# Optimization experiments

Hardware: AMD Instinct MI355X
Metric: run time of the kernel (lower is better)

## Reference

```python
import jax, jax.numpy as jnp
import numpy as np

N = 50000        # n_nodes
F_IN = 256       # features_size
E_DIM = 128      # embedding_size
K = 2
N_FILT = 5
N_EDGES = 600000
EPS = 1e-9


def setup_inputs() -> dict:
    key = jax.random.key(0)
    ks = jax.random.split(key, 12)
    stdv = 1.0 / np.sqrt(E_DIM)  # matches torch reset_parameters / nn.Linear init scale
    feature = jax.random.normal(ks[0], (N, F_IN), dtype=jnp.float32)
    edge_index = jax.random.randint(ks[1], (2, N_EDGES), 0, N, dtype=jnp.int64)
    edge_weight = jax.random.uniform(ks[2], (N_EDGES,), dtype=jnp.float32)
    weight = jax.random.normal(ks[3], (F_IN, E_DIM), dtype=jnp.float32) * stdv
    low_gamma = jax.random.uniform(ks[4], (N_FILT, K), dtype=jnp.float32)
    mid_gamma = jax.random.uniform(ks[5], (N_FILT, K), dtype=jnp.float32)
    q_w = jax.random.normal(ks[6], (E_DIM, E_DIM), dtype=jnp.float32) * stdv
    q_b = jax.random.normal(ks[7], (E_DIM,), dtype=jnp.float32) * stdv
    k_w = jax.random.normal(ks[8], (E_DIM, E_DIM), dtype=jnp.float32) * stdv
    k_b = jax.random.normal(ks[9], (E_DIM,), dtype=jnp.float32) * stdv
    v_w = jax.random.normal(ks[10], (E_DIM, E_DIM), dtype=jnp.float32) * stdv
    v_b = jax.random.normal(ks[11], (E_DIM,), dtype=jnp.float32) * stdv
    return {"feature": feature, "edge_index": edge_index, "edge_weight": edge_weight,
            "weight": weight, "low_gamma": low_gamma, "mid_gamma": mid_gamma,
            "q_w": q_w, "q_b": q_b, "k_w": k_w, "k_b": k_b, "v_w": v_w, "v_b": v_b}


def reference(feature, edge_index, edge_weight, weight, low_gamma, mid_gamma,
              q_w, q_b, k_w, k_b, v_w, v_b):
    n = feature.shape[0]
    support = jax.nn.relu(feature @ weight)                     # [N, E]
    row, col = edge_index[0], edge_index[1]
    # torch.spmm(adj, support): adj_support[i] = sum_e w_e * support[col_e] for row_e == i
    adj_support = jax.ops.segment_sum(edge_weight[:, None] * support[col], row,
                                      num_segments=n)           # [N, E]

    alpha = jnp.linspace(jnp.float32(-EPS), jnp.float32(1.0 + EPS), K)  # [K]

    # low filters: out_i = dot(alpha, g_i) * adj_support + dot(1-alpha, g_i) * support, summed over i
    gl = jax.nn.relu(low_gamma)                                 # [5, K]
    a_low = jnp.sum(gl @ alpha)
    b_low = jnp.sum(gl @ (1.0 - alpha))
    output_low = a_low * adj_support + b_low * support          # [N, E]

    # mid filters: out_i = sum(g_i) * adj_support - dot(alpha, g_i) * support, summed over i
    gm = jax.nn.relu(mid_gamma)
    a_mid = jnp.sum(gm)
    c_mid = jnp.sum(gm @ alpha)
    output_mid = a_mid * adj_support - c_mid * support          # [N, E]

    # SelfAttention over the 2 filter outputs per node
    x = jnp.stack([output_low, output_mid], axis=1)             # [N, 2, E]
    q = x @ q_w.T + q_b
    k = x @ k_w.T + k_b
    v = x @ v_w.T + v_b
    scores = jnp.einsum('nqe,nke->nqk', q, k) / jnp.sqrt(jnp.float32(E_DIM))
    # NOTE: original uses nn.Softmax(dim=1) -> softmax over the QUERY axis
    w = jax.nn.softmax(scores, axis=1)                          # [N, 2, 2]
    context = jnp.einsum('nqk,nke->nqe', w, v)                  # [N, 2, E]
    return jnp.sum(context, axis=1)                             # [N, E]
```

## Files before the change

### kernel.cpp

```cpp
#include <hip/hip_runtime.h>
#include <hip/hip_bf16.h>

static constexpr int EDIM = 128;
static constexpr int FIN  = 256;
static constexpr int CAP  = 64;

typedef __attribute__((ext_vector_type(8))) short bf16x8;
typedef __attribute__((ext_vector_type(4))) float f32x4;

__device__ inline short f2b(float f) {
    __hip_bfloat16 h = __float2bfloat16(f);
    return *reinterpret_cast<short*>(&h);
}

__global__ __launch_bounds__(256) void k_prep(const float* __restrict__ W,
                                              const float* __restrict__ vw,
                                              const float* __restrict__ lg,
                                              const float* __restrict__ mg,
                                              short* __restrict__ WtF,
                                              short* __restrict__ vwF,
                                              float* __restrict__ sc,
                                              int* __restrict__ cnt, int M) {
    const int bid = blockIdx.x, tid = threadIdx.x;
    if (bid < 16) {
        int idx = bid * 256 + tid;
        int kt = idx >> 9, rem = idx & 511;
        int nf = rem >> 6, lane = rem & 63;
        int l15 = lane & 15, lhi = lane >> 4;
        bf16x8 fr;
        #pragma unroll
        for (int i = 0; i < 8; ++i)
            fr[i] = f2b(W[(size_t)(kt*32 + lhi*8 + i) * EDIM + nf*16 + l15]);
        *(bf16x8*)(WtF + (size_t)idx * 8) = fr;
    } else if (bid < 24) {
        int idx = (bid - 16) * 256 + tid;
        int ks = idx >> 9, rem = idx & 511;
        int nf = rem >> 6, lane = rem & 63;
        int l15 = lane & 15, lhi = lane >> 4;
        bf16x8 fr;
        #pragma unroll
        for (int i = 0; i < 8; ++i)
            fr[i] = f2b(vw[(size_t)(nf*16 + l15) * EDIM + ks*32 + lhi*8 + i]);
        *(bf16x8*)(vwF + (size_t)idx * 8) = fr;
    } else if (bid == 24) {
        if (tid == 0) {
            const float a0 = -1e-9f, a1 = 1.0f + 1e-9f;
            float a_low = 0.f, b_low = 0.f, a_mid = 0.f, c_mid = 0.f;
            for (int i = 0; i < 5; ++i) {
                float l0 = fmaxf(lg[2*i], 0.f), l1 = fmaxf(lg[2*i+1], 0.f);
                a_low += l0 * a0 + l1 * a1;
                b_low += l0 * (1.f - a0) + l1 * (1.f - a1);
                float m0 = fmaxf(mg[2*i], 0.f), m1 = fmaxf(mg[2*i+1], 0.f);
                a_mid += m0 + m1;
                c_mid += m0 * a0 + m1 * a1;
            }
            sc[0] = a_low + a_mid;
            sc[1] = b_low - c_mid;
        }
    } else {
        int i = (bid - 25) * 256 + tid;
        if (i < M) cnt[i] = 0;
    }
}

__global__ __launch_bounds__(256) void k_mega(const float* __restrict__ F,
                                              const short* __restrict__ WtF,
                                              const short* __restrict__ vwF,
                                              short* __restrict__ Yb,
                                              const int* __restrict__ ei,
                                              const float* __restrict__ ew,
                                              int* __restrict__ cnt,
                                              int2* __restrict__ colw,
                                              int M, int ne, int R, int nFill) {
    __shared__ short L[32768];
    const int gGemm = (M + 63) >> 6;
    const int bid = blockIdx.x, tid = threadIdx.x;

    if (bid >= gGemm) {
        int bid2 = bid - gGemm;
        int part = bid2 & 7;
        int lo = part * R, hi = lo + R;
        int stride = (nFill >> 3) * 256;
        for (int e = (bid2 >> 3) * 256 + tid; e < ne; e += stride) {
            int r = ei[e];
            if (r >= lo && r < hi) {
                int pos = atomicAdd(&cnt[r], 1);
                if (pos < CAP)
                    colw[(size_t)r * CAP + pos] =
                        make_int2(ei[ne + e], __float_as_int(ew[e]));
            }
        }
        return;
    }

    const int wave = tid >> 6, lane = tid & 63;
    const int l15  = lane & 15, lhi = lane >> 4;
    const int bm   = bid * 64;
    const int wrow = wave * 16;

    {
        const int4* src = (const int4*)WtF;
        int4* dst = (int4*)L;
        #pragma unroll 4
        for (int i = 0; i < 16; ++i) {
            int idx = tid + i * 256;
            dst[idx] = src[idx];
        }
    }
    __syncthreads();

    const int gr_a = bm + wrow + l15;
    const bool va  = gr_a < M;
    const float* fp = F + (size_t)(va ? gr_a : 0) * FIN + lhi * 8;

    f32x4 acc[8];
    #pragma unroll
    for (int b = 0; b < 8; ++b) acc[b] = (f32x4){0.f, 0.f, 0.f, 0.f};

    float4 c0 = make_float4(0.f,0.f,0.f,0.f), c1 = c0;
    if (va) { c0 = *(const float4*)(fp); c1 = *(const float4*)(fp + 4); }
    #pragma unroll
    for (int kt = 0; kt < 8; ++kt) {
        float4 n0 = make_float4(0.f,0.f,0.f,0.f), n1 = n0;
        if (kt < 7 && va) {
            n0 = *(const float4*)(fp + (kt+1)*32);
            n1 = *(const float4*)(fp + (kt+1)*32 + 4);
        }
        bf16x8 af;
        af[0]=f2b(c0.x); af[1]=f2b(c0.y); af[2]=f2b(c0.z); af[3]=f2b(c0.w);
        af[4]=f2b(c1.x); af[5]=f2b(c1.y); af[6]=f2b(c1.z); af[7]=f2b(c1.w);
        #pragma unroll
        for (int nf = 0; nf < 8; ++nf) {
            bf16x8 bf = *(const bf16x8*)(&L[((kt*8 + nf)*64 + lane) * 8]);
            acc[nf] = __builtin_amdgcn_mfma_f32_16x16x32_bf16(af, bf, acc[nf], 0, 0, 0);
        }
        c0 = n0; c1 = n1;
    }
    __syncthreads();

    {
        const int4* src = (const int4*)vwF;
        int4* dst = (int4*)(L + 8704);
        #pragma unroll 4
        for (int i = 0; i < 8; ++i) {
            int idx = tid + i * 256;
            dst[idx] = src[idx];
        }
    }
    #pragma unroll
    for (int nf = 0; nf < 8; ++nf)
        #pragma unroll
        for (int i = 0; i < 4; ++i)
            L[(wrow + lhi*4 + i) * 136 + nf*16 + l15] = f2b(fmaxf(acc[nf][i], 0.f));
    __syncthreads();

    f32x4 acc2[8];
    #pragma unroll
    for (int b = 0; b < 8; ++b) acc2[b] = (f32x4){0.f, 0.f, 0.f, 0.f};

    #pragma unroll
    for (int ks = 0; ks < 4; ++ks) {
        bf16x8 af2 = *(const bf16x8*)(&L[(wrow + l15) * 136 + ks*32 + lhi*8]);
        #pragma unroll
        for (int nf = 0; nf < 8; ++nf) {
            bf16x8 bf2 = *(const bf16x8*)(&L[8704 + ((ks*8 + nf)*64 + lane) * 8]);
            acc2[nf] = __builtin_amdgcn_mfma_f32_16x16x32_bf16(af2, bf2, acc2[nf], 0, 0, 0);
        }
    }

    #pragma unroll
    for (int nf = 0; nf < 8; ++nf)
        #pragma unroll
        for (int i = 0; i < 4; ++i)
            L[(wrow + lhi*4 + i) * 136 + nf*16 + l15] = f2b(acc2[nf][i]);

    const int srow = lane >> 2;
    const int sch  = (lane & 3) * 32;
    const int gr_s = bm + wrow + srow;
    if (gr_s < M) {
        #pragma unroll
        for (int r = 0; r < 4; ++r) {
            float4 t = *(const float4*)(&L[(wrow + srow) * 136 + sch + r*8]);
            *(float4*)(Yb + (size_t)gr_s * EDIM + sch + r*8) = t;
        }
    }
}

__global__ __launch_bounds__(256) void k_gather(const int2* __restrict__ colw,
                                                const int* __restrict__ cnt,
                                                const __hip_bfloat162* __restrict__ Yb,
                                                const float* __restrict__ vb,
                                                const float* __restrict__ sc,
                                                float* __restrict__ out, int n) {
    int row  = (blockIdx.x * blockDim.x + threadIdx.x) >> 6;
    int lane = threadIdx.x & 63;
    if (row >= n) return;
    int c = __builtin_amdgcn_readfirstlane(cnt[row]);
    if (c > CAP) c = CAP;
    const int2* bucket = colw + (size_t)row * CAP;
    const float Aa = sc[0];
    const float Bb = sc[1];

    float2 acc = make_float2(0.f, 0.f);
    int j = 0;
    for (; j + 8 <= c; j += 8) {
        float2 v[8]; float w[8];
        #pragma unroll
        for (int u = 0; u < 8; ++u) {
            int2 e = bucket[j + u];
            w[u] = __int_as_float(e.y);
            v[u] = __bfloat1622float2(Yb[(size_t)e.x * 64 + lane]);
        }
        #pragma unroll
        for (int u = 0; u < 8; ++u) {
            acc.x = fmaf(w[u], v[u].x, acc.x);
            acc.y = fmaf(w[u], v[u].y, acc.y);
        }
    }
    for (; j + 4 <= c; j += 4) {
        float2 v[4]; float w[4];
        #pragma unroll
        for (int u = 0; u < 4; ++u) {
            int2 e = bucket[j + u];
            w[u] = __int_as_float(e.y);
            v[u] = __bfloat1622float2(Yb[(size_t)e.x * 64 + lane]);
        }
        #pragma unroll
        for (int u = 0; u < 4; ++u) {
            acc.x = fmaf(w[u], v[u].x, acc.x);
            acc.y = fmaf(w[u], v[u].y, acc.y);
        }
    }
    for (; j < c; ++j) {
        int2 e = bucket[j];
        float w = __int_as_float(e.y);
        float2 v = __bfloat1622float2(Yb[(size_t)e.x * 64 + lane]);
        acc.x = fmaf(w, v.x, acc.x);
        acc.y = fmaf(w, v.y, acc.y);
    }
    float2 y = __bfloat1622float2(Yb[(size_t)row * 64 + lane]);
    float2 b = *(const float2*)(vb + lane * 2);
    float2 o;
    o.x = fmaf(Aa, acc.x, fmaf(Bb, y.x, 2.f * b.x));
    o.y = fmaf(Aa, acc.y, fmaf(Bb, y.y, 2.f * b.y));
    *(float2*)(out + (size_t)row * EDIM + lane * 2) = o;
}

extern "C" void kernel_launch(void* const* d_in, const int* in_sizes, int n_in,
                              void* d_out, int out_size, void* d_ws, size_t ws_size,
                              hipStream_t stream) {
    const float* feature = (const float*)d_in[0];
    const int*   eidx    = (const int*)d_in[1];
    const float* ew      = (const float*)d_in[2];
    const float* weight  = (const float*)d_in[3];
    const float* lg      = (const float*)d_in[4];
    const float* mg      = (const float*)d_in[5];
    const float* vw      = (const float*)d_in[10];
    const float* vb      = (const float*)d_in[11];
    float* out = (float*)d_out;

    const int M  = in_sizes[0] / FIN;
    const int NE = in_sizes[2];

    char* ws = (char*)d_ws;
    short* Yb   = (short*)ws;
    char* p = ws + (size_t)M * EDIM * 2;
    int2*  colw = (int2*)p;          p += (size_t)M * CAP * 8;
    int*   cnt  = (int*)p;           p += (size_t)M * 4;
    short* WtF  = (short*)p;         p += (size_t)EDIM * FIN * 2;
    short* vwF  = (short*)p;         p += (size_t)EDIM * EDIM * 2;
    float* sc   = (float*)p;

    const int nb = (M + 255) / 256;
    const int R  = (M + 7) / 8;
    const int NFILL = 2048;

    k_prep<<<25 + nb, 256, 0, stream>>>(weight, vw, lg, mg, WtF, vwF, sc, cnt, M);

    const int gGemm = (M + 63) / 64;
    k_mega<<<gGemm + NFILL, 256, 0, stream>>>(feature, WtF, vwF, Yb,
                                              eidx, ew, cnt, colw, M, NE, R, NFILL);

    int gGather = ((M * 64) + 255) / 256;
    k_gather<<<gGather, 256, 0, stream>>>(colw, cnt, (const __hip_bfloat162*)Yb,
                                          vb, sc, out, M);
}
```

Baseline: 101.4 us.

## Pack edge buckets into 32-bit entries and read GEMM weights from global

Each edge bucket entry is now one 32-bit word: the column index in the upper 16 bits and the edge weight as bf16 in the lower 16. This halves bucket write and read traffic in the fill and gather phases. Separately, the mega kernel no longer stages the bf16 weight matrices in LDS. MFMA B fragments are loaded straight from global memory, which shrinks shared memory to one 64x136 tile, drops several barriers and should raise occupancy. The trade-offs are that the packing only works for fewer than 65536 nodes, edge weights lose precision, and weight fragments now depend on cache hits instead of LDS.

```diff
diff --git a/kernel.cpp b/kernel.cpp
--- a/kernel.cpp
+++ b/kernel.cpp
@@ -70,9 +70,9 @@
                                               const int* __restrict__ ei,
                                               const float* __restrict__ ew,
                                               int* __restrict__ cnt,
-                                              int2* __restrict__ colw,
+                                              unsigned* __restrict__ bkt,
                                               int M, int ne, int R, int nFill) {
-    __shared__ short L[32768];
+    __shared__ short Sb[64 * 136];
     const int gGemm = (M + 63) >> 6;
     const int bid = blockIdx.x, tid = threadIdx.x;
 
@@ -85,9 +85,11 @@
             int r = ei[e];
             if (r >= lo && r < hi) {
                 int pos = atomicAdd(&cnt[r], 1);
-                if (pos < CAP)
-                    colw[(size_t)r * CAP + pos] =
-                        make_int2(ei[ne + e], __float_as_int(ew[e]));
+                if (pos < CAP) {
+                    unsigned pk = ((unsigned)ei[ne + e] << 16) |
+                                  (unsigned short)f2b(ew[e]);
+                    bkt[(size_t)r * CAP + pos] = pk;
+                }
             }
         }
         return;
@@ -97,17 +99,6 @@
     const int l15  = lane & 15, lhi = lane >> 4;
     const int bm   = bid * 64;
     const int wrow = wave * 16;
-
-    {
-        const int4* src = (const int4*)WtF;
-        int4* dst = (int4*)L;
-        #pragma unroll 4
-        for (int i = 0; i < 16; ++i) {
-            int idx = tid + i * 256;
-            dst[idx] = src[idx];
-        }
-    }
-    __syncthreads();
 
     const int gr_a = bm + wrow + l15;
     const bool va  = gr_a < M;
@@ -131,28 +122,17 @@
         af[4]=f2b(c1.x); af[5]=f2b(c1.y); af[6]=f2b(c1.z); af[7]=f2b(c1.w);
         #pragma unroll
         for (int nf = 0; nf < 8; ++nf) {
-            bf16x8 bf = *(const bf16x8*)(&L[((kt*8 + nf)*64 + lane) * 8]);
+            bf16x8 bf = *(const bf16x8*)(WtF + (size_t)((kt*8 + nf)*64 + lane) * 8);
             acc[nf] = __builtin_amdgcn_mfma_f32_16x16x32_bf16(af, bf, acc[nf], 0, 0, 0);
         }
         c0 = n0; c1 = n1;
     }
-    __syncthreads();
-
-    {
-        const int4* src = (const int4*)vwF;
-        int4* dst = (int4*)(L + 8704);
-        #pragma unroll 4
-        for (int i = 0; i < 8; ++i) {
-            int idx = tid + i * 256;
-            dst[idx] = src[idx];
-        }
-    }
+
     #pragma unroll
     for (int nf = 0; nf < 8; ++nf)
         #pragma unroll
         for (int i = 0; i < 4; ++i)
-            L[(wrow + lhi*4 + i) * 136 + nf*16 + l15] = f2b(fmaxf(acc[nf][i], 0.f));
-    __syncthreads();
+            Sb[(wrow + lhi*4 + i) * 136 + nf*16 + l15] = f2b(fmaxf(acc[nf][i], 0.f));
 
     f32x4 acc2[8];
     #pragma unroll
@@ -160,10 +140,10 @@
 
     #pragma unroll
     for (int ks = 0; ks < 4; ++ks) {
-        bf16x8 af2 = *(const bf16x8*)(&L[(wrow + l15) * 136 + ks*32 + lhi*8]);
+        bf16x8 af2 = *(const bf16x8*)(&Sb[(wrow + l15) * 136 + ks*32 + lhi*8]);
         #pragma unroll
         for (int nf = 0; nf < 8; ++nf) {
-            bf16x8 bf2 = *(const bf16x8*)(&L[8704 + ((ks*8 + nf)*64 + lane) * 8]);
+            bf16x8 bf2 = *(const bf16x8*)(vwF + (size_t)((ks*8 + nf)*64 + lane) * 8);
             acc2[nf] = __builtin_amdgcn_mfma_f32_16x16x32_bf16(af2, bf2, acc2[nf], 0, 0, 0);
         }
     }
@@ -172,7 +152,7 @@
     for (int nf = 0; nf < 8; ++nf)
         #pragma unroll
         for (int i = 0; i < 4; ++i)
-            L[(wrow + lhi*4 + i) * 136 + nf*16 + l15] = f2b(acc2[nf][i]);
+            Sb[(wrow + lhi*4 + i) * 136 + nf*16 + l15] = f2b(acc2[nf][i]);
 
     const int srow = lane >> 2;
     const int sch  = (lane & 3) * 32;
@@ -180,13 +160,13 @@
     if (gr_s < M) {
         #pragma unroll
         for (int r = 0; r < 4; ++r) {
-            float4 t = *(const float4*)(&L[(wrow + srow) * 136 + sch + r*8]);
+            float4 t = *(const float4*)(&Sb[(wrow + srow) * 136 + sch + r*8]);
             *(float4*)(Yb + (size_t)gr_s * EDIM + sch + r*8) = t;
         }
     }
 }
 
-__global__ __launch_bounds__(256) void k_gather(const int2* __restrict__ colw,
+__global__ __launch_bounds__(256) void k_gather(const unsigned* __restrict__ bkt,
                                                 const int* __restrict__ cnt,
                                                 const __hip_bfloat162* __restrict__ Yb,
                                                 const float* __restrict__ vb,
@@ -197,7 +177,7 @@
     if (row >= n) return;
     int c = __builtin_amdgcn_readfirstlane(cnt[row]);
     if (c > CAP) c = CAP;
-    const int2* bucket = colw + (size_t)row * CAP;
+    const unsigned* bucket = bkt + (size_t)row * CAP;
     const float Aa = sc[0];
     const float Bb = sc[1];
 
@@ -207,9 +187,9 @@
         float2 v[8]; float w[8];
         #pragma unroll
         for (int u = 0; u < 8; ++u) {
-            int2 e = bucket[j + u];
-            w[u] = __int_as_float(e.y);
-            v[u] = __bfloat1622float2(Yb[(size_t)e.x * 64 + lane]);
+            unsigned e = bucket[j + u];
+            w[u] = __uint_as_float(e << 16);
+            v[u] = __bfloat1622float2(Yb[(size_t)(e >> 16) * 64 + lane]);
         }
         #pragma unroll
         for (int u = 0; u < 8; ++u) {
@@ -221,9 +201,9 @@
         float2 v[4]; float w[4];
         #pragma unroll
         for (int u = 0; u < 4; ++u) {
-            int2 e = bucket[j + u];
-            w[u] = __int_as_float(e.y);
-            v[u] = __bfloat1622float2(Yb[(size_t)e.x * 64 + lane]);
+            unsigned e = bucket[j + u];
+            w[u] = __uint_as_float(e << 16);
+            v[u] = __bfloat1622float2(Yb[(size_t)(e >> 16) * 64 + lane]);
         }
         #pragma unroll
         for (int u = 0; u < 4; ++u) {
@@ -232,9 +212,9 @@
         }
     }
     for (; j < c; ++j) {
-        int2 e = bucket[j];
-        float w = __int_as_float(e.y);
-        float2 v = __bfloat1622float2(Yb[(size_t)e.x * 64 + lane]);
+        unsigned e = bucket[j];
+        float w = __uint_as_float(e << 16);
+        float2 v = __bfloat1622float2(Yb[(size_t)(e >> 16) * 64 + lane]);
         acc.x = fmaf(w, v.x, acc.x);
         acc.y = fmaf(w, v.y, acc.y);
     }
@@ -263,13 +243,13 @@
     const int NE = in_sizes[2];
 
     char* ws = (char*)d_ws;
-    short* Yb   = (short*)ws;
+    short* Yb      = (short*)ws;
     char* p = ws + (size_t)M * EDIM * 2;
-    int2*  colw = (int2*)p;          p += (size_t)M * CAP * 8;
-    int*   cnt  = (int*)p;           p += (size_t)M * 4;
-    short* WtF  = (short*)p;         p += (size_t)EDIM * FIN * 2;
-    short* vwF  = (short*)p;         p += (size_t)EDIM * EDIM * 2;
-    float* sc   = (float*)p;
+    unsigned* bkt  = (unsigned*)p;   p += (size_t)M * CAP * 4;
+    int*   cnt     = (int*)p;        p += (size_t)M * 4;
+    short* WtF     = (short*)p;      p += (size_t)EDIM * FIN * 2;
+    short* vwF     = (short*)p;      p += (size_t)EDIM * EDIM * 2;
+    float* sc      = (float*)p;
 
     const int nb = (M + 255) / 256;
     const int R  = (M + 7) / 8;
@@ -279,9 +259,9 @@
 
     const int gGemm = (M + 63) / 64;
     k_mega<<<gGemm + NFILL, 256, 0, stream>>>(feature, WtF, vwF, Yb,
-                                              eidx, ew, cnt, colw, M, NE, R, NFILL);
+                                              eidx, ew, cnt, bkt, M, NE, R, NFILL);
 
     int gGather = ((M * 64) + 255) / 256;
-    k_gather<<<gGather, 256, 0, stream>>>(colw, cnt, (const __hip_bfloat162*)Yb,
+    k_gather<<<gGather, 256, 0, stream>>>(bkt, cnt, (const __hip_bfloat162*)Yb,
                                           vb, sc, out, M);
 }
```

After: 86.01 us. -15.1%, faster.
